# Performance work log

Measured on AMD Instinct MI355X. Metric: run time of the kernel, lower is better.

Reference implementation:

```python
import jax, jax.numpy as jnp
import numpy as np

EPS = 1e-8  # torch.cosine_similarity default eps (applied per-norm clamp)


def setup_inputs() -> dict:
    key = jax.random.key(0)
    k1, k2, k3 = jax.random.split(key, 3)
    B, D = 8192, 4096
    ques = jax.random.normal(k1, (B, D), dtype=jnp.float32)
    ans = jax.random.normal(k2, (B, D), dtype=jnp.float32)
    # labels in {-1, +1}, shape [B, 1] as in the torch module
    label = (2 * jax.random.randint(k3, (B, 1), 0, 2) - 1).astype(jnp.int32)
    margin = 0.5  # scalar hinge margin
    return {"ques": ques, "ans": ans, "label": label, "margin": margin}


def reference(ques, ans, label, margin):
    # Per-row cosine similarity (torch semantics: each norm clamped to eps)
    qn = jnp.maximum(jnp.linalg.norm(ques, axis=-1), EPS)  # [B]
    an = jnp.maximum(jnp.linalg.norm(ans, axis=-1), EPS)   # [B]
    cos = jnp.sum(ques * ans, axis=-1) / (qn * an)          # [B]

    lab = label[:, 0]
    mask_true = lab == 1
    mask_false = lab == -1

    true_ave = jnp.sum(jnp.where(mask_true, cos, 0.0)) / jnp.sum(mask_true)
    false_ave = jnp.sum(jnp.where(mask_false, cos, 0.0)) / jnp.sum(mask_false)

    loss = jnp.maximum(0.0, margin - true_ave + false_ave)
    return loss.reshape(1)  # torch version returns a shape-[1] tensor
```

## Files before the change

kernel.cpp:

```cpp
#include <hip/hip_runtime.h>

#define D_DIM 4096
#define EPSF 1e-8f

__global__ __launch_bounds__(256) void cosim_rows(const float* __restrict__ q,
                                                  const float* __restrict__ a,
                                                  float* __restrict__ cos_out) {
    const int row = blockIdx.x;
    const int t = threadIdx.x;
    const float4* q4 = reinterpret_cast<const float4*>(q + (size_t)row * D_DIM);
    const float4* a4 = reinterpret_cast<const float4*>(a + (size_t)row * D_DIM);

    float dot = 0.f, qq = 0.f, aa = 0.f;
#pragma unroll
    for (int k = 0; k < 4; ++k) {
        float4 vq = q4[t + k * 256];
        float4 va = a4[t + k * 256];
        dot += vq.x * va.x + vq.y * va.y + vq.z * va.z + vq.w * va.w;
        qq  += vq.x * vq.x + vq.y * vq.y + vq.z * vq.z + vq.w * vq.w;
        aa  += va.x * va.x + va.y * va.y + va.z * va.z + va.w * va.w;
    }

#pragma unroll
    for (int off = 32; off > 0; off >>= 1) {
        dot += __shfl_down(dot, off, 64);
        qq  += __shfl_down(qq,  off, 64);
        aa  += __shfl_down(aa,  off, 64);
    }

    __shared__ float s[3][4];
    const int wave = t >> 6;
    if ((t & 63) == 0) { s[0][wave] = dot; s[1][wave] = qq; s[2][wave] = aa; }
    __syncthreads();
    if (t == 0) {
        float d   = s[0][0] + s[0][1] + s[0][2] + s[0][3];
        float qsq = s[1][0] + s[1][1] + s[1][2] + s[1][3];
        float asq = s[2][0] + s[2][1] + s[2][2] + s[2][3];
        float qn = fmaxf(sqrtf(qsq), EPSF);
        float an = fmaxf(sqrtf(asq), EPSF);
        cos_out[row] = d / (qn * an);
    }
}

__global__ __launch_bounds__(256) void cosim_finalize(const float* __restrict__ cosv,
                                                      const int* __restrict__ label,
                                                      const float* __restrict__ margin,
                                                      float* __restrict__ out, int B) {
    const int t = threadIdx.x;
    float ts = 0.f, fs = 0.f, tc = 0.f, fc = 0.f;
    for (int i = t; i < B; i += 256) {
        float c = cosv[i];
        int l = label[i];
        if (l == 1)       { ts += c; tc += 1.f; }
        else if (l == -1) { fs += c; fc += 1.f; }
    }
#pragma unroll
    for (int off = 32; off > 0; off >>= 1) {
        ts += __shfl_down(ts, off, 64);
        fs += __shfl_down(fs, off, 64);
        tc += __shfl_down(tc, off, 64);
        fc += __shfl_down(fc, off, 64);
    }
    __shared__ float s[4][4];
    const int wave = t >> 6;
    if ((t & 63) == 0) { s[0][wave] = ts; s[1][wave] = fs; s[2][wave] = tc; s[3][wave] = fc; }
    __syncthreads();
    if (t == 0) {
        float tsum = s[0][0] + s[0][1] + s[0][2] + s[0][3];
        float fsum = s[1][0] + s[1][1] + s[1][2] + s[1][3];
        float tcnt = s[2][0] + s[2][1] + s[2][2] + s[2][3];
        float fcnt = s[3][0] + s[3][1] + s[3][2] + s[3][3];
        float true_ave  = tsum / tcnt;
        float false_ave = fsum / fcnt;
        out[0] = fmaxf(0.f, margin[0] - true_ave + false_ave);
    }
}

extern "C" void kernel_launch(void* const* d_in, const int* in_sizes, int n_in,
                              void* d_out, int out_size, void* d_ws, size_t ws_size,
                              hipStream_t stream) {
    const float* ques   = (const float*)d_in[0];
    const float* ans    = (const float*)d_in[1];
    const int*   label  = (const int*)d_in[2];
    const float* margin = (const float*)d_in[3];
    float* out = (float*)d_out;

    const int B = in_sizes[2];
    float* cosv = (float*)d_ws;

    cosim_rows<<<B, 256, 0, stream>>>(ques, ans, cosv);
    cosim_finalize<<<1, 256, 0, stream>>>(cosv, label, margin, out, B);
}
```

Before: 62.01 us.

## Map one wavefront per row instead of one block per row

Result: no change. 61.69 us (-0.5%).

```diff
diff --git a/kernel.cpp b/kernel.cpp
--- a/kernel.cpp
+++ b/kernel.cpp
@@ -3,19 +3,22 @@
 #define D_DIM 4096
 #define EPSF 1e-8f
 
+typedef float f32x4 __attribute__((ext_vector_type(4)));
+
 __global__ __launch_bounds__(256) void cosim_rows(const float* __restrict__ q,
                                                   const float* __restrict__ a,
-                                                  float* __restrict__ cos_out) {
-    const int row = blockIdx.x;
-    const int t = threadIdx.x;
-    const float4* q4 = reinterpret_cast<const float4*>(q + (size_t)row * D_DIM);
-    const float4* a4 = reinterpret_cast<const float4*>(a + (size_t)row * D_DIM);
+                                                  float* __restrict__ cosv) {
+    const int row  = (blockIdx.x * 256 + threadIdx.x) >> 6;
+    const int lane = threadIdx.x & 63;
+
+    const f32x4* q4 = reinterpret_cast<const f32x4*>(q + (size_t)row * D_DIM);
+    const f32x4* a4 = reinterpret_cast<const f32x4*>(a + (size_t)row * D_DIM);
 
     float dot = 0.f, qq = 0.f, aa = 0.f;
 #pragma unroll
-    for (int k = 0; k < 4; ++k) {
-        float4 vq = q4[t + k * 256];
-        float4 va = a4[t + k * 256];
+    for (int k = 0; k < 16; ++k) {
+        f32x4 vq = q4[lane + k * 64];
+        f32x4 va = a4[lane + k * 64];
         dot += vq.x * va.x + vq.y * va.y + vq.z * va.z + vq.w * va.w;
         qq  += vq.x * vq.x + vq.y * vq.y + vq.z * vq.z + vq.w * vq.w;
         aa  += va.x * va.x + va.y * va.y + va.z * va.z + va.w * va.w;
@@ -28,17 +31,10 @@
         aa  += __shfl_down(aa,  off, 64);
     }
 
-    __shared__ float s[3][4];
-    const int wave = t >> 6;
-    if ((t & 63) == 0) { s[0][wave] = dot; s[1][wave] = qq; s[2][wave] = aa; }
-    __syncthreads();
-    if (t == 0) {
-        float d   = s[0][0] + s[0][1] + s[0][2] + s[0][3];
-        float qsq = s[1][0] + s[1][1] + s[1][2] + s[1][3];
-        float asq = s[2][0] + s[2][1] + s[2][2] + s[2][3];
-        float qn = fmaxf(sqrtf(qsq), EPSF);
-        float an = fmaxf(sqrtf(asq), EPSF);
-        cos_out[row] = d / (qn * an);
+    if (lane == 0) {
+        float qn = fmaxf(sqrtf(qq), EPSF);
+        float an = fmaxf(sqrtf(aa), EPSF);
+        cosv[row] = dot / (qn * an);
     }
 }
 
@@ -70,9 +66,7 @@
         float fsum = s[1][0] + s[1][1] + s[1][2] + s[1][3];
         float tcnt = s[2][0] + s[2][1] + s[2][2] + s[2][3];
         float fcnt = s[3][0] + s[3][1] + s[3][2] + s[3][3];
-        float true_ave  = tsum / tcnt;
-        float false_ave = fsum / fcnt;
-        out[0] = fmaxf(0.f, margin[0] - true_ave + false_ave);
+        out[0] = fmaxf(0.f, margin[0] - tsum / tcnt + fsum / fcnt);
     }
 }
 
@@ -88,6 +82,6 @@
     const int B = in_sizes[2];
     float* cosv = (float*)d_ws;
 
-    cosim_rows<<<B, 256, 0, stream>>>(ques, ans, cosv);
+    cosim_rows<<<B / 4, 256, 0, stream>>>(ques, ans, cosv);
     cosim_finalize<<<1, 256, 0, stream>>>(cosv, label, margin, out, B);
 }
```
